# Optimization experiments

Hardware: AMD Instinct MI355X
Metric: run time of the kernel (lower is better)

Reference implementation:

```python
import jax, jax.numpy as jnp
import numpy as np

N = 100000      # nodes
E = 400000      # directed edges
G = 2048        # graphs in batch
DIN = 128       # input atom-feature dim
RANK = 256      # hidden dim
NLAYER = 3
EPS = 1e-5      # BatchNorm eps


def gcn_conv(h, W, b, src, dst):
    # PyG GCNConv: x @ W, add self-loops, D^{-1/2} A_hat D^{-1/2} aggregation, + bias
    hw = h @ W                                   # [N, rank]
    loop = jnp.arange(N)
    s = jnp.concatenate([src, loop])             # [E+N]
    d = jnp.concatenate([dst, loop])
    deg = jax.ops.segment_sum(jnp.ones(s.shape[0], hw.dtype), d, num_segments=N)
    dinv = jnp.where(deg > 0, deg ** -0.5, 0.0)
    norm = dinv[s] * dinv[d]                     # [E+N]
    out = jax.ops.segment_sum(norm[:, None] * hw[s], d, num_segments=N)
    return out + b


def batchnorm(h, gamma, beta):
    # BatchNorm1d in training mode: batch statistics over node dim
    mu = h.mean(axis=0)
    var = h.var(axis=0)
    return gamma * (h - mu) * jax.lax.rsqrt(var + EPS) + beta


def global_max_pool(h, batch):
    out = jax.ops.segment_max(h, batch, num_segments=G)
    # guard rare empty graphs (-inf init) -> 0
    return jnp.where(jnp.isfinite(out), out, 0.0)


def setup_inputs() -> dict:
    key = jax.random.key(0)
    ks = jax.random.split(key, 10)
    x = jax.random.normal(ks[0], (N, DIN), dtype=jnp.float32)
    edge_index = jax.random.randint(ks[1], (2, E), 0, N, dtype=jnp.int64)
    batch = jnp.sort(jax.random.randint(ks[2], (N,), 0, G, dtype=jnp.int64))
    inp = {"x": x, "edge_index": edge_index, "batch": batch}
    dims = [DIN, RANK, RANK]
    for i in range(NLAYER):
        scale = 1.0 / np.sqrt(dims[i])
        inp[f"W{i}"] = jax.random.normal(ks[3 + i], (dims[i], RANK), dtype=jnp.float32) * scale
        inp[f"b{i}"] = jnp.zeros((RANK,), dtype=jnp.float32)
        inp[f"gamma{i}"] = jnp.ones((RANK,), dtype=jnp.float32)
        inp[f"beta{i}"] = jnp.zeros((RANK,), dtype=jnp.float32)
    return inp


def reference(x, edge_index, batch,
              W0, b0, gamma0, beta0,
              W1, b1, gamma1, beta1,
              W2, b2, gamma2, beta2):
    src, dst = edge_index[0], edge_index[1]
    params = [(W0, b0, gamma0, beta0), (W1, b1, gamma1, beta1), (W2, b2, gamma2, beta2)]
    h = x
    outs = []
    for (W, b, g, be) in params:
        h = batchnorm(jnp.tanh(gcn_conv(h, W, b, src, dst)), g, be)
        outs.append(global_max_pool(h, batch))    # [G, RANK]
    return tuple(outs)
```

## Files before the change

### kernel.cpp

```cpp
#include <hip/hip_runtime.h>
#include <hip/hip_bf16.h>
#include <math.h>

#define NN 100000
#define NE 400000
#define NG 2048
#define BN_EPS 1e-5f
#define NB_SCAN 98

typedef short short8 __attribute__((ext_vector_type(8)));
typedef float f32x4 __attribute__((ext_vector_type(4)));
typedef unsigned short u16x4 __attribute__((ext_vector_type(4)));
typedef unsigned short u16x8 __attribute__((ext_vector_type(8)));

__device__ __forceinline__ float bf2f(unsigned short u){
  union { unsigned u; float f; } x; x.u = ((unsigned)u) << 16; return x.f;
}
__device__ __forceinline__ unsigned short f2bf(float f){
  union { float f; unsigned u; } x; x.f = f;
  unsigned r = x.u + 0x7FFFu + ((x.u >> 16) & 1u);
  return (unsigned short)(r >> 16);
}

__global__ void k_zero(float* p, long n){
  long i = (long)blockIdx.x * blockDim.x + threadIdx.x;
  if (i < n) p[i] = 0.f;
}

__global__ void k_deg(const int* __restrict__ dst, int* __restrict__ deg){
  int e = blockIdx.x * blockDim.x + threadIdx.x;
  if (e < NE) atomicAdd(&deg[dst[e]], 1);
}

__global__ void k_scan1(const int* __restrict__ deg, int* __restrict__ bsum,
                        float* __restrict__ dinv){
  __shared__ int s[256];
  int b = blockIdx.x, t = threadIdx.x;
  int base = b * 1024;
  int v = 0;
  #pragma unroll
  for (int i = 0; i < 4; ++i){
    int idx = base + t + i * 256;
    if (idx < NN){
      int d = deg[idx];
      v += d;
      dinv[idx] = rsqrtf((float)(d + 1));
    }
  }
  s[t] = v; __syncthreads();
  for (int o = 128; o; o >>= 1){
    if (t < o) s[t] += s[t + o];
    __syncthreads();
  }
  if (t == 0) bsum[b] = s[0];
}

__global__ void k_scan2(const int* __restrict__ bsum, int* __restrict__ boff){
  __shared__ int s[128];
  int t = threadIdx.x;
  int v = (t < NB_SCAN) ? bsum[t] : 0;
  s[t] = v; __syncthreads();
  for (int o = 1; o < 128; o <<= 1){
    int x = (t >= o) ? s[t - o] : 0;
    __syncthreads();
    s[t] += x;
    __syncthreads();
  }
  if (t < NB_SCAN) boff[t] = s[t] - v;
}

__global__ void k_scan3(const int* __restrict__ deg, const int* __restrict__ boff,
                        int* __restrict__ rowptr, int* __restrict__ cursor){
  __shared__ int s[256];
  int b = blockIdx.x, t = threadIdx.x;
  int base = b * 1024 + t * 4;
  int d[4]; int loc = 0;
  #pragma unroll
  for (int i = 0; i < 4; ++i){
    int idx = base + i;
    d[i] = (idx < NN) ? deg[idx] : 0;
    loc += d[i];
  }
  s[t] = loc; __syncthreads();
  for (int o = 1; o < 256; o <<= 1){
    int x = (t >= o) ? s[t - o] : 0;
    __syncthreads();
    s[t] += x;
    __syncthreads();
  }
  int run = boff[b] + s[t] - loc;
  #pragma unroll
  for (int i = 0; i < 4; ++i){
    int idx = base + i;
    if (idx < NN){ rowptr[idx] = run; cursor[idx] = run; run += d[i]; }
  }
  if (b == NB_SCAN - 1 && t == 255) rowptr[NN] = run;
}

__global__ void k_fill(const int* __restrict__ src, const int* __restrict__ dst,
                       const float* __restrict__ dinv, int* __restrict__ cursor,
                       int2* __restrict__ csr){
  int e = blockIdx.x * blockDim.x + threadIdx.x;
  if (e >= NE) return;
  int s = src[e], d = dst[e];
  int p = atomicAdd(&cursor[d], 1);
  csr[p] = make_int2(s, __float_as_int(dinv[s]));
}

__global__ void k_bounds(const int* __restrict__ batch, int* __restrict__ start){
  int i = blockIdx.x * blockDim.x + threadIdx.x;
  if (i >= NN) return;
  int cur = batch[i];
  int prev = (i == 0) ? -1 : batch[i - 1];
  for (int g = prev + 1; g <= cur; ++g) start[g] = i;
  if (i == NN - 1) for (int g = cur + 1; g <= NG; ++g) start[g] = NN;
}

__global__ void k_copybias(const float* __restrict__ b0, const float* __restrict__ b1,
                           const float* __restrict__ b2, float* __restrict__ dst){
  int c = threadIdx.x;
  dst[c] = b0[c];
  dst[256 + c] = b1[c];
  dst[512 + c] = b2[c];
}

__global__ void k_repack3(const float* __restrict__ W0, const float* __restrict__ W1,
                          const float* __restrict__ W2,
                          unsigned short* __restrict__ Wp0,
                          float* __restrict__ Wf32){
  int gid = blockIdx.x * blockDim.x + threadIdx.x;
  if (gid >= 20480) return;
  const float* W; int f; int layer;
  if (gid < 4096){ W = W0; f = gid; layer = 0; }
  else if (gid < 12288){ W = W1; f = gid - 4096; layer = 1; }
  else { W = W2; f = gid - 12288; layer = 2; }
  int l = f & 63, t = (f >> 6) & 15, kb = f >> 10;
  int q = l >> 4, m = l & 15;
  if (layer == 0){
    unsigned short* o = Wp0 + (size_t)f * 8;
    #pragma unroll
    for (int j = 0; j < 8; ++j)
      o[j] = f2bf(W[(size_t)(kb * 32 + q * 8 + j) * 256 + t * 16 + m]);
  } else {
    float* o = Wf32 + (size_t)(layer - 1) * 65536 + (size_t)f * 8;
    #pragma unroll
    for (int j = 0; j < 8; ++j)
      o[j] = W[(size_t)(kb * 32 + q * 8 + j) * 256 + t * 16 + m];
  }
}

__global__ void k_bncoef(const float* __restrict__ gsum, const float* __restrict__ gsumsq,
                         const float* __restrict__ gamma,
                         const float* __restrict__ beta,
                         const float* __restrict__ Wnext,
                         float* __restrict__ coefA, float* __restrict__ coefB,
                         float* __restrict__ bias2){
  __shared__ float sb[256];
  __shared__ float part[4][256];
  int t = threadIdx.x;
  int c = t & 255, kq = t >> 8;
  if (kq == 0){
    float mu = gsum[c] * (1.f / NN);
    float var = gsumsq[c] * (1.f / NN) - mu * mu;
    float a = gamma[c] / sqrtf(var + BN_EPS);
    coefA[c] = a;
    float b = beta[c] - mu * a;
    coefB[c] = b;
    sb[c] = b;
  }
  if (Wnext == nullptr) return;
  __syncthreads();
  float acc = 0.f;
  #pragma unroll 8
  for (int k = kq * 64; k < kq * 64 + 64; ++k)
    acc += sb[k] * Wnext[(size_t)k * 256 + c];
  part[kq][c] = acc;
  __syncthreads();
  if (kq == 0)
    bias2[c] = part[0][c] + part[1][c] + part[2][c] + part[3][c];
}

__global__ void k_wprep(const float* __restrict__ Wf32, const float* __restrict__ coefA,
                        unsigned short* __restrict__ WpS){
  int gid = blockIdx.x * blockDim.x + threadIdx.x;
  if (gid >= 8192) return;
  int l = gid & 63, kb = gid >> 10;
  int q = l >> 4;
  int k0 = kb * 32 + q * 8;
  const float* wf = Wf32 + (size_t)gid * 8;
  unsigned short* o = WpS + (size_t)gid * 8;
  #pragma unroll
  for (int j = 0; j < 8; ++j)
    o[j] = f2bf(coefA[k0 + j] * wf[j]);
}

#define STAGE_WP8(SRC, KB, BUF) do {                                            \
    const char* gsrc_ = (const char*)(SRC) + (size_t)(KB) * 16384 + wave * 2048 \
                        + lane * 16;                                            \
    char* ldst_ = (char*)(&sW[(BUF)][0]) + wave * 2048;                         \
    _Pragma("unroll")                                                           \
    for (int c_ = 0; c_ < 2; ++c_)                                              \
      __builtin_amdgcn_global_load_lds(                                         \
        (const __attribute__((address_space(1))) void*)(gsrc_ + c_ * 1024),     \
        (__attribute__((address_space(3))) void*)(ldst_ + c_ * 1024),           \
        16, 0, 0);                                                              \
  } while (0)

__global__ __launch_bounds__(512) void k_gemm0(const float* __restrict__ A,
                                               const unsigned short* __restrict__ Wp,
                                               unsigned short* __restrict__ out){
  const int K = 128;
  __shared__ unsigned short sW[2][8192];
  int lane = threadIdx.x & 63;
  int wave = threadIdx.x >> 6;
  int m0 = blockIdx.x * 128 + wave * 16;
  int q = lane >> 4, m = lane & 15;
  int arow = m0 + m;
  bool valid = arow < NN;
  const float* ap = A + (size_t)arow * K + q * 8;
  f32x4 areg[8];
  if (valid){
    #pragma unroll
    for (int kb = 0; kb < 4; ++kb){
      areg[2 * kb]     = *(const f32x4*)(ap + kb * 32);
      areg[2 * kb + 1] = *(const f32x4*)(ap + kb * 32 + 4);
    }
  }
  f32x4 acc[16] = {};
  STAGE_WP8(Wp, 0, 0);
  __syncthreads();
  int buf = 0;
  for (int kb = 0; kb < 4; ++kb){
    if (kb < 3) STAGE_WP8(Wp, kb + 1, buf ^ 1);
    short8 ahi = {}, alo = {};
    if (valid){
      float xs[8] = {areg[2*kb][0], areg[2*kb][1], areg[2*kb][2], areg[2*kb][3],
                     areg[2*kb+1][0], areg[2*kb+1][1], areg[2*kb+1][2], areg[2*kb+1][3]};
      #pragma unroll
      for (int j = 0; j < 8; ++j){
        unsigned short h = f2bf(xs[j]);
        ahi[j] = (short)h;
        alo[j] = (short)f2bf(xs[j] - bf2f(h));
      }
    }
    #pragma unroll
    for (int t = 0; t < 16; ++t){
      short8 b = *(const short8*)(&sW[buf][t * 512 + lane * 8]);
      acc[t] = __builtin_amdgcn_mfma_f32_16x16x32_bf16(ahi, b, acc[t], 0, 0, 0);
      acc[t] = __builtin_amdgcn_mfma_f32_16x16x32_bf16(alo, b, acc[t], 0, 0, 0);
    }
    __syncthreads();
    buf ^= 1;
  }
  int r0 = m0 + q * 4;
  #pragma unroll
  for (int t = 0; t < 16; ++t)
    #pragma unroll
    for (int r = 0; r < 4; ++r){
      int row = r0 + r;
      if (row < NN) out[(size_t)row * 256 + t * 16 + m] = f2bf(acc[t][r]);
    }
}

__global__ __launch_bounds__(512) void k_gemm12(const unsigned short* __restrict__ A,
                                                const unsigned short* __restrict__ Wp,
                                                const float* __restrict__ bias2,
                                                unsigned short* __restrict__ out){
  const int K = 256;
  __shared__ unsigned short sW[2][8192];
  __shared__ float sb2[256];
  if (threadIdx.x < 256) sb2[threadIdx.x] = bias2[threadIdx.x];
  int lane = threadIdx.x & 63;
  int wave = threadIdx.x >> 6;
  int m0 = blockIdx.x * 128 + wave * 16;
  int q = lane >> 4, m = lane & 15;
  int arow = m0 + m;
  bool valid = arow < NN;
  const unsigned short* ap = A + (size_t)arow * K + q * 8;
  short8 areg[8] = {};
  if (valid){
    #pragma unroll
    for (int kb = 0; kb < 8; ++kb) areg[kb] = *(const short8*)(ap + kb * 32);
  }
  f32x4 acc[16] = {};
  STAGE_WP8(Wp, 0, 0);
  __syncthreads();
  int buf = 0;
  for (int kb = 0; kb < 8; ++kb){
    if (kb < 7) STAGE_WP8(Wp, kb + 1, buf ^ 1);
    #pragma unroll
    for (int t = 0; t < 16; ++t){
      short8 b = *(const short8*)(&sW[buf][t * 512 + lane * 8]);
      acc[t] = __builtin_amdgcn_mfma_f32_16x16x32_bf16(areg[kb], b, acc[t], 0, 0, 0);
    }
    __syncthreads();
    buf ^= 1;
  }
  int r0 = m0 + q * 4;
  #pragma unroll
  for (int t = 0; t < 16; ++t){
    float b2 = sb2[t * 16 + m];
    #pragma unroll
    for (int r = 0; r < 4; ++r){
      int row = r0 + r;
      if (row < NN) out[(size_t)row * 256 + t * 16 + m] = f2bf(acc[t][r] + b2);
    }
  }
}

__global__ __launch_bounds__(256) void k_gather(const int* __restrict__ rowptr,
                                                const int2* __restrict__ csr,
                                                const float* __restrict__ dinv,
                                                const unsigned short* __restrict__ B,
                                                const float* __restrict__ bias,
                                                unsigned short* __restrict__ C,
                                                float* __restrict__ gsum,
                                                float* __restrict__ gsumsq){
  __shared__ float lsum[4][256];
  __shared__ float lss[4][256];
  int lane = threadIdx.x & 63;
  int wv = threadIdx.x >> 6;
  int hl = lane & 31;
  int c8 = hl * 8;
  int gs = (int)((blockIdx.x * 256 + threadIdx.x) >> 5);
  int ns = (int)((gridDim.x * 256) >> 5);
  f32x4 bia0 = *(const f32x4*)(bias + c8);
  f32x4 bia1 = *(const f32x4*)(bias + c8 + 4);
  f32x4 s0 = {}, s1 = {}, ss0 = {}, ss1 = {};
  int v = gs;
  float dv_n = 0.f; int e_n = 0, e1_n = 0; u16x8 bv_n = {};
  if (v < NN){
    dv_n = dinv[v];
    e_n = rowptr[v];
    e1_n = rowptr[v + 1];
    bv_n = *(const u16x8*)(B + (size_t)v * 256 + c8);
  }
  while (v < NN){
    float dv = dv_n;
    int e = e_n, e1 = e1_n;
    u16x8 bv = bv_n;
    int vn = v + ns;
    if (vn < NN){
      dv_n = dinv[vn];
      e_n = rowptr[vn];
      e1_n = rowptr[vn + 1];
      bv_n = *(const u16x8*)(B + (size_t)vn * 256 + c8);
    }
    float a[8], a2[8];
    #pragma unroll
    for (int j = 0; j < 8; ++j){ a[j] = dv * bf2f(bv[j]); a2[j] = 0.f; }
    if (e1 - e >= 2){
      int2 Ea = csr[e], Eb = csr[e + 1];
      u16x8 ra = *(const u16x8*)(B + (size_t)Ea.x * 256 + c8);
      u16x8 rb = *(const u16x8*)(B + (size_t)Eb.x * 256 + c8);
      float wa = __int_as_float(Ea.y), wb = __int_as_float(Eb.y);
      e += 2;
      while (e + 1 < e1){
        int2 Ec = csr[e], Ed = csr[e + 1];
        u16x8 rc = *(const u16x8*)(B + (size_t)Ec.x * 256 + c8);
        u16x8 rd = *(const u16x8*)(B + (size_t)Ed.x * 256 + c8);
        #pragma unroll
        for (int j = 0; j < 8; ++j){
          a[j]  += wa * bf2f(ra[j]);
          a2[j] += wb * bf2f(rb[j]);
        }
        ra = rc; rb = rd;
        wa = __int_as_float(Ec.y); wb = __int_as_float(Ed.y);
        e += 2;
      }
      #pragma unroll
      for (int j = 0; j < 8; ++j){
        a[j]  += wa * bf2f(ra[j]);
        a2[j] += wb * bf2f(rb[j]);
      }
    }
    if (e < e1){
      int2 Ee = csr[e];
      u16x8 re = *(const u16x8*)(B + (size_t)Ee.x * 256 + c8);
      float we = __int_as_float(Ee.y);
      #pragma unroll
      for (int j = 0; j < 8; ++j) a[j] += we * bf2f(re[j]);
    }
    u16x8 ct;
    #pragma unroll
    for (int j = 0; j < 8; ++j){
      float bj = (j < 4) ? bia0[j] : bia1[j - 4];
      float t = tanhf(dv * (a[j] + a2[j]) + bj);
      ct[j] = f2bf(t);
      if (j < 4){ s0[j] += t; ss0[j] += t * t; }
      else      { s1[j - 4] += t; ss1[j - 4] += t * t; }
    }
    *(u16x8*)(C + (size_t)v * 256 + c8) = ct;
    v = vn;
  }
  #pragma unroll
  for (int j = 0; j < 4; ++j){
    s0[j]  += __shfl_xor(s0[j], 32);
    s1[j]  += __shfl_xor(s1[j], 32);
    ss0[j] += __shfl_xor(ss0[j], 32);
    ss1[j] += __shfl_xor(ss1[j], 32);
  }
  if ((lane >> 5) == 0){
    *(f32x4*)(&lsum[wv][c8])     = s0;
    *(f32x4*)(&lsum[wv][c8 + 4]) = s1;
    *(f32x4*)(&lss[wv][c8])      = ss0;
    *(f32x4*)(&lss[wv][c8 + 4])  = ss1;
  }
  __syncthreads();
  if (wv == 0){
    int c4 = lane * 4;
    f32x4 aa = *(f32x4*)(&lsum[0][c4]);
    f32x4 bb = *(f32x4*)(&lss[0][c4]);
    #pragma unroll
    for (int w2 = 1; w2 < 4; ++w2){
      aa += *(f32x4*)(&lsum[w2][c4]);
      bb += *(f32x4*)(&lss[w2][c4]);
    }
    #pragma unroll
    for (int i = 0; i < 4; ++i){
      atomicAdd(&gsum[c4 + i], aa[i]);
      atomicAdd(&gsumsq[c4 + i], bb[i]);
    }
  }
}

__global__ __launch_bounds__(256) void k_pool(const unsigned short* __restrict__ C,
                                              const int* __restrict__ start,
                                              const float* __restrict__ coefA,
                                              const float* __restrict__ coefB,
                                              float* __restrict__ out){
  __shared__ float smx[4][256];
  __shared__ float smn[4][256];
  int g = blockIdx.x;
  int w = threadIdx.x >> 6, lane = threadIdx.x & 63;
  int c4 = lane * 4;
  int s = start[g], e = start[g + 1];
  float mx[4] = {-INFINITY, -INFINITY, -INFINITY, -INFINITY};
  float mn[4] = { INFINITY,  INFINITY,  INFINITY,  INFINITY};
  for (int row = s + w; row < e; row += 4){
    u16x4 v = *(const u16x4*)(C + (size_t)row * 256 + c4);
    #pragma unroll
    for (int j = 0; j < 4; ++j){
      float f = bf2f(v[j]);
      mx[j] = fmaxf(mx[j], f);
      mn[j] = fminf(mn[j], f);
    }
  }
  #pragma unroll
  for (int j = 0; j < 4; ++j){
    smx[w][c4 + j] = mx[j];
    smn[w][c4 + j] = mn[j];
  }
  __syncthreads();
  if (w == 0){
    #pragma unroll
    for (int j = 0; j < 4; ++j){
      int c = c4 + j;
      float M = fmaxf(fmaxf(smx[0][c], smx[1][c]), fmaxf(smx[2][c], smx[3][c]));
      float m = fminf(fminf(smn[0][c], smn[1][c]), fminf(smn[2][c], smn[3][c]));
      float a = coefA[c], b = coefB[c];
      float r = (a >= 0.f) ? (a * M + b) : (a * m + b);
      out[(size_t)g * 256 + c] = (e > s) ? r : 0.f;
    }
  }
}

extern "C" void kernel_launch(void* const* d_in, const int* in_sizes, int n_in,
                              void* d_out, int out_size, void* d_ws, size_t ws_size,
                              hipStream_t stream){
  const float* x = (const float*)d_in[0];
  const int* eidx = (const int*)d_in[1];
  const int* batch = (const int*)d_in[2];
  const int* src  = eidx;
  const int* dstv = eidx + NE;
  const float* W[3]  = {(const float*)d_in[3],  (const float*)d_in[7],  (const float*)d_in[11]};
  const float* bb[3] = {(const float*)d_in[4],  (const float*)d_in[8],  (const float*)d_in[12]};
  const float* gm[3] = {(const float*)d_in[5],  (const float*)d_in[9],  (const float*)d_in[13]};
  const float* bt[3] = {(const float*)d_in[6],  (const float*)d_in[10], (const float*)d_in[14]};
  float* out = (float*)d_out;

  char* w = (char*)d_ws;
  unsigned short* B = (unsigned short*)w; w += (size_t)NN * 256 * 2;
  unsigned short* C = (unsigned short*)w; w += (size_t)NN * 256 * 2;
  int2* csr = (int2*)w;            w += (size_t)NE * 8;
  float* dinv = (float*)w;         w += (size_t)NN * 4;
  int* deg = (int*)w;              w += (size_t)NN * 4;
  int* rowptr = (int*)w;           w += (size_t)(NN + 4) * 4;
  int* cursor = (int*)w;           w += (size_t)NN * 4;
  int* bsum = (int*)w;             w += (size_t)128 * 4;
  int* boff = (int*)w;             w += (size_t)128 * 4;
  unsigned short* Wp0 = (unsigned short*)w; w += (size_t)32768 * 2;
  float* Wf32 = (float*)w;         w += (size_t)131072 * 4;
  unsigned short* WpS = (unsigned short*)w; w += (size_t)65536 * 2;
  float* stat = (float*)w;         w += (size_t)3 * 512 * 4;
  float* coefA = (float*)w;        w += 256 * 4;
  float* coefB = (float*)w;        w += 256 * 4;
  float* bias2 = (float*)w;        w += 256 * 4;
  float* biasws = (float*)w;       w += (size_t)3 * 256 * 4;
  int* start = (int*)w;            w += (size_t)(NG + 1) * 4;

  k_zero<<<(NN + 255) / 256, 256, 0, stream>>>((float*)deg, NN);
  k_zero<<<6, 256, 0, stream>>>(stat, 3 * 512);
  k_deg<<<(NE + 255) / 256, 256, 0, stream>>>(dstv, deg);
  k_scan1<<<NB_SCAN, 256, 0, stream>>>(deg, bsum, dinv);
  k_scan2<<<1, 128, 0, stream>>>(bsum, boff);
  k_scan3<<<NB_SCAN, 256, 0, stream>>>(deg, boff, rowptr, cursor);
  k_fill<<<(NE + 255) / 256, 256, 0, stream>>>(src, dstv, dinv, cursor, csr);
  k_bounds<<<(NN + 255) / 256, 256, 0, stream>>>(batch, start);
  k_repack3<<<80, 256, 0, stream>>>(W[0], W[1], W[2], Wp0, Wf32);
  k_copybias<<<1, 256, 0, stream>>>(bb[0], bb[1], bb[2], biasws);

  for (int L = 0; L < 3; ++L){
    float* gsumL = stat + (size_t)L * 512;
    float* gsumsqL = gsumL + 256;
    if (L == 0){
      k_gemm0<<<(NN + 127) / 128, 512, 0, stream>>>(x, Wp0, B);
    } else {
      k_gemm12<<<(NN + 127) / 128, 512, 0, stream>>>(C, WpS, bias2, B);
    }
    k_gather<<<512, 256, 0, stream>>>(rowptr, csr, dinv, B,
                                      biasws + (size_t)L * 256,
                                      C, gsumL, gsumsqL);
    k_bncoef<<<1, 1024, 0, stream>>>(gsumL, gsumsqL, gm[L], bt[L],
                                     (L < 2) ? W[L + 1] : nullptr,
                                     coefA, coefB, bias2);
    if (L < 2)
      k_wprep<<<32, 256, 0, stream>>>(Wf32 + (size_t)L * 65536, coefA, WpS);
    k_pool<<<NG, 256, 0, stream>>>(C, start, coefA, coefB,
                                   out + (size_t)L * NG * 256);
  }
}
```

Measured before the change: 673.7 us.

## Process gather nodes in degree-sorted order to balance wavefront work

Builds a counting-sort permutation of nodes by in-degree (capped at 63) using histogram, scan and scatter kernels. The gather kernel then visits nodes through this permutation, so the half-wave groups that run together see similar edge counts and diverge less. It adds three small setup kernels and an extra indirection per node. The output row writes become scattered instead of sequential, and within each degree bucket the node order is nondeterministic because of the atomic scatter. The workspace is reordered so deg, stat and hist sit next to each other and one zero kernel clears all three.

```diff
diff --git a/kernel.cpp b/kernel.cpp
--- a/kernel.cpp
+++ b/kernel.cpp
@@ -30,6 +30,26 @@
 __global__ void k_deg(const int* __restrict__ dst, int* __restrict__ deg){
   int e = blockIdx.x * blockDim.x + threadIdx.x;
   if (e < NE) atomicAdd(&deg[dst[e]], 1);
+}
+
+__global__ void k_hist(const int* __restrict__ deg, int* __restrict__ hist){
+  int v = blockIdx.x * blockDim.x + threadIdx.x;
+  if (v < NN) atomicAdd(&hist[min(deg[v], 63)], 1);
+}
+
+__global__ void k_hscan(int* __restrict__ hist){
+  if (threadIdx.x == 0){
+    int run = 0;
+    for (int i = 0; i < 64; ++i){ int h = hist[i]; hist[i] = run; run += h; }
+  }
+}
+
+__global__ void k_scatter(const int* __restrict__ deg, int* __restrict__ hist,
+                          int* __restrict__ perm){
+  int v = blockIdx.x * blockDim.x + threadIdx.x;
+  if (v >= NN) return;
+  int pos = atomicAdd(&hist[min(deg[v], 63)], 1);
+  perm[pos] = v;
 }
 
 __global__ void k_scan1(const int* __restrict__ deg, int* __restrict__ bsum,
@@ -308,7 +328,8 @@
   }
 }
 
-__global__ __launch_bounds__(256) void k_gather(const int* __restrict__ rowptr,
+__global__ __launch_bounds__(256) void k_gather(const int* __restrict__ perm,
+                                                const int* __restrict__ rowptr,
                                                 const int2* __restrict__ csr,
                                                 const float* __restrict__ dinv,
                                                 const unsigned short* __restrict__ B,
@@ -327,24 +348,27 @@
   f32x4 bia0 = *(const f32x4*)(bias + c8);
   f32x4 bia1 = *(const f32x4*)(bias + c8 + 4);
   f32x4 s0 = {}, s1 = {}, ss0 = {}, ss1 = {};
-  int v = gs;
-  float dv_n = 0.f; int e_n = 0, e1_n = 0; u16x8 bv_n = {};
-  if (v < NN){
-    dv_n = dinv[v];
-    e_n = rowptr[v];
-    e1_n = rowptr[v + 1];
-    bv_n = *(const u16x8*)(B + (size_t)v * 256 + c8);
-  }
-  while (v < NN){
+  int idx = gs;
+  int v_n = 0; float dv_n = 0.f; int e_n = 0, e1_n = 0; u16x8 bv_n = {};
+  if (idx < NN){
+    v_n = perm[idx];
+    dv_n = dinv[v_n];
+    e_n = rowptr[v_n];
+    e1_n = rowptr[v_n + 1];
+    bv_n = *(const u16x8*)(B + (size_t)v_n * 256 + c8);
+  }
+  while (idx < NN){
+    int v = v_n;
     float dv = dv_n;
     int e = e_n, e1 = e1_n;
     u16x8 bv = bv_n;
-    int vn = v + ns;
-    if (vn < NN){
-      dv_n = dinv[vn];
-      e_n = rowptr[vn];
-      e1_n = rowptr[vn + 1];
-      bv_n = *(const u16x8*)(B + (size_t)vn * 256 + c8);
+    int in2 = idx + ns;
+    if (in2 < NN){
+      v_n = perm[in2];
+      dv_n = dinv[v_n];
+      e_n = rowptr[v_n];
+      e1_n = rowptr[v_n + 1];
+      bv_n = *(const u16x8*)(B + (size_t)v_n * 256 + c8);
     }
     float a[8], a2[8];
     #pragma unroll
@@ -391,7 +415,7 @@
       else      { s1[j - 4] += t; ss1[j - 4] += t * t; }
     }
     *(u16x8*)(C + (size_t)v * 256 + c8) = ct;
-    v = vn;
+    idx = in2;
   }
   #pragma unroll
   for (int j = 0; j < 4; ++j){
@@ -483,25 +507,29 @@
   unsigned short* B = (unsigned short*)w; w += (size_t)NN * 256 * 2;
   unsigned short* C = (unsigned short*)w; w += (size_t)NN * 256 * 2;
   int2* csr = (int2*)w;            w += (size_t)NE * 8;
+  int* deg = (int*)w;              w += (size_t)NN * 4;
+  float* stat = (float*)w;         w += (size_t)3 * 512 * 4;
+  int* hist = (int*)w;             w += (size_t)64 * 4;
   float* dinv = (float*)w;         w += (size_t)NN * 4;
-  int* deg = (int*)w;              w += (size_t)NN * 4;
   int* rowptr = (int*)w;           w += (size_t)(NN + 4) * 4;
   int* cursor = (int*)w;           w += (size_t)NN * 4;
+  int* perm = (int*)w;             w += (size_t)NN * 4;
   int* bsum = (int*)w;             w += (size_t)128 * 4;
   int* boff = (int*)w;             w += (size_t)128 * 4;
   unsigned short* Wp0 = (unsigned short*)w; w += (size_t)32768 * 2;
   float* Wf32 = (float*)w;         w += (size_t)131072 * 4;
   unsigned short* WpS = (unsigned short*)w; w += (size_t)65536 * 2;
-  float* stat = (float*)w;         w += (size_t)3 * 512 * 4;
   float* coefA = (float*)w;        w += 256 * 4;
   float* coefB = (float*)w;        w += 256 * 4;
   float* bias2 = (float*)w;        w += 256 * 4;
   float* biasws = (float*)w;       w += (size_t)3 * 256 * 4;
   int* start = (int*)w;            w += (size_t)(NG + 1) * 4;
 
-  k_zero<<<(NN + 255) / 256, 256, 0, stream>>>((float*)deg, NN);
-  k_zero<<<6, 256, 0, stream>>>(stat, 3 * 512);
+  k_zero<<<(NN + 1536 + 64 + 255) / 256, 256, 0, stream>>>((float*)deg, NN + 1536 + 64);
   k_deg<<<(NE + 255) / 256, 256, 0, stream>>>(dstv, deg);
+  k_hist<<<(NN + 255) / 256, 256, 0, stream>>>(deg, hist);
+  k_hscan<<<1, 64, 0, stream>>>(hist);
+  k_scatter<<<(NN + 255) / 256, 256, 0, stream>>>(deg, hist, perm);
   k_scan1<<<NB_SCAN, 256, 0, stream>>>(deg, bsum, dinv);
   k_scan2<<<1, 128, 0, stream>>>(bsum, boff);
   k_scan3<<<NB_SCAN, 256, 0, stream>>>(deg, boff, rowptr, cursor);
@@ -518,7 +546,7 @@
     } else {
       k_gemm12<<<(NN + 127) / 128, 512, 0, stream>>>(C, WpS, bias2, B);
     }
-    k_gather<<<512, 256, 0, stream>>>(rowptr, csr, dinv, B,
+    k_gather<<<512, 256, 0, stream>>>(perm, rowptr, csr, dinv, B,
                                       biasws + (size_t)L * 256,
                                       C, gsumL, gsumsqL);
     k_bncoef<<<1, 1024, 0, stream>>>(gsumL, gsumsqL, gm[L], bt[L],
```

Result: slower. 1.436 ms (+113.2%).
